# Performance work log

Measured on AMD Instinct MI355X. Metric: run time of the kernel, lower is better.

## Reference

```python
import jax, jax.numpy as jnp
import numpy as np

B, S, HID = 1, 2048, 2560
H, HKV, D = 32, 8, 128
G = H // HKV  # GQA group size = 4
EPS = 1e-6
THETA = 1000000.0


def _make_freqs_cis(seq_len, dim, theta):
    inv_freq = 1.0 / (theta ** (np.arange(0, dim, 2, dtype=np.float32) / dim))
    t = np.arange(seq_len, dtype=np.float32)
    ang = np.outer(t, inv_freq)  # [S, D/2]
    emb = np.concatenate([ang, ang], axis=-1)  # [S, D]
    return jnp.asarray(np.stack([np.cos(emb), np.sin(emb)], axis=0))  # [2, S, D]


def setup_inputs() -> dict:
    key = jax.random.key(0)
    ks = jax.random.split(key, 5)
    inp = {
        "hidden_states": jax.random.normal(ks[0], (B, S, HID), dtype=jnp.float32),
        "freqs_cis": _make_freqs_cis(S, D, THETA),
        "Wq": jax.random.normal(ks[1], (H * D, HID), dtype=jnp.float32) * 0.02,
        "Wk": jax.random.normal(ks[2], (HKV * D, HID), dtype=jnp.float32) * 0.02,
        "Wv": jax.random.normal(ks[3], (HKV * D, HID), dtype=jnp.float32) * 0.02,
        "Wo": jax.random.normal(ks[4], (HID, H * D), dtype=jnp.float32) * 0.02,
        "q_norm_w": jnp.ones((D,), dtype=jnp.float32),
        "k_norm_w": jnp.ones((D,), dtype=jnp.float32),
    }
    return inp


def _rms_norm(x, w):
    var = jnp.mean(jnp.square(x), axis=-1, keepdims=True)
    return x * jax.lax.rsqrt(var + EPS) * w


def _rotate_half(x):
    x1, x2 = jnp.split(x, 2, axis=-1)
    return jnp.concatenate([-x2, x1], axis=-1)


def reference(hidden_states, freqs_cis, Wq, Wk, Wv, Wo, q_norm_w, k_norm_w):
    # projections (torch Linear: x @ W.T)
    xq = jnp.einsum('bsh,oh->bso', hidden_states, Wq).reshape(B, S, H, D).swapaxes(1, 2)   # [B,H,S,D]
    xk = jnp.einsum('bsh,oh->bso', hidden_states, Wk).reshape(B, S, HKV, D).swapaxes(1, 2) # [B,Hkv,S,D]
    xv = jnp.einsum('bsh,oh->bso', hidden_states, Wv).reshape(B, S, HKV, D).swapaxes(1, 2)

    # per-head RMSNorm (gemma3-style q/k norm)
    xq = _rms_norm(xq, q_norm_w)
    xk = _rms_norm(xk, k_norm_w)

    # RoPE; cos/sin: [S,D] broadcasts over [B,H,S,D]
    cos, sin = freqs_cis[0], freqs_cis[1]
    xq = xq * cos + _rotate_half(xq) * sin
    xk = xk * cos + _rotate_half(xk) * sin

    # GQA attention without materializing repeated KV: group queries per kv head
    qg = xq.reshape(B, HKV, G, S, D)
    scores = jnp.einsum('bkgqd,bksd->bkgqs', qg, xk) / jnp.sqrt(jnp.asarray(D, xq.dtype))
    probs = jax.nn.softmax(scores, axis=-1)
    out = jnp.einsum('bkgqs,bksd->bkgqd', probs, xv)  # [B,Hkv,G,S,D]

    out = out.reshape(B, H, S, D).swapaxes(1, 2).reshape(B, S, H * D)
    return jnp.einsum('bso,ho->bsh', out, Wo)
```

## Files before the change

kernel.cpp:

```cpp
#include <hip/hip_runtime.h>
#include <stdint.h>

#define S_LEN 2048
#define HID   2560
#define NH    32
#define NKV   8
#define DH    128
#define QD    (NH*DH)
#define KVD   (NKV*DH)

typedef __attribute__((ext_vector_type(8)))  short          bf16x8;
typedef __attribute__((ext_vector_type(4)))  float          f32x4;
typedef __attribute__((ext_vector_type(16))) float          f32x16;
typedef __attribute__((ext_vector_type(8)))  unsigned short us8;

static __device__ __forceinline__ unsigned short f2bf(float f) {
  union { float f; uint32_t u; } v; v.f = f;
  uint32_t u = v.u;
  u += 0x7fff + ((u >> 16) & 1);
  return (unsigned short)(u >> 16);
}

static __device__ __forceinline__ void gload16(const void* g, void* l) {
  __builtin_amdgcn_global_load_lds(
      (const __attribute__((address_space(1))) uint32_t*)g,
      (__attribute__((address_space(3))) uint32_t*)l, 16, 0, 0);
}

static __device__ __forceinline__ unsigned cvtpk(float lo, float hi) {
  unsigned r;
  asm volatile("v_cvt_pk_bf16_f32 %0, %1, %2" : "=v"(r) : "v"(lo), "v"(hi));
  return r;
}

static __device__ __forceinline__ void plswap(unsigned& a, unsigned& b) {
  asm volatile("v_permlane32_swap_b32 %0, %1" : "+v"(a), "+v"(b));
}

__global__ void cast_bf16_k(const float* __restrict__ in,
                            unsigned short* __restrict__ out, int n4) {
  int stride = gridDim.x * blockDim.x;
  for (int i = blockIdx.x * blockDim.x + threadIdx.x; i < n4; i += stride) {
    float4 v = ((const float4*)in)[i];
    ushort4 o;
    o.x = f2bf(v.x); o.y = f2bf(v.y); o.z = f2bf(v.z); o.w = f2bf(v.w);
    ((ushort4*)out)[i] = o;
  }
}

#define BM 128
#define BN 128
#define BK 32

__global__ __launch_bounds__(256)
void gemm_bt(const unsigned short* __restrict__ A,
             const unsigned short* __restrict__ B,
             float* __restrict__ Cf, int M, int N, int K)
{
  __shared__ __align__(16) unsigned short sA[BM * BK];
  __shared__ __align__(16) unsigned short sB[BN * BK];
  const int tid  = threadIdx.x;
  const int wave = tid >> 6, lane = tid & 63;
  const int wr   = wave >> 1, wc = wave & 1;
  const int brow = blockIdx.y, bcol = blockIdx.x;
  const int l15  = lane & 15, lh = lane >> 4;

  f32x4 acc[4][4] = {};

  for (int k0 = 0; k0 < K; k0 += BK) {
    __syncthreads();
#pragma unroll
    for (int c = 0; c < 2; ++c) {
      int chunk = wave * 2 + c;
      int f = chunk * 512 + lane * 8;
      int row = f >> 5, col = f & 31;
      gload16(A + (size_t)(brow * BM + row) * K + k0 + col, (char*)sA + chunk * 1024);
      gload16(B + (size_t)(bcol * BN + row) * K + k0 + col, (char*)sB + chunk * 1024);
    }
    __syncthreads();

    bf16x8 af[4], bfr[4];
#pragma unroll
    for (int i = 0; i < 4; ++i)
      af[i] = *(const bf16x8*)((const char*)sA + (wr * 64 + i * 16 + l15) * 64 + lh * 16);
#pragma unroll
    for (int j = 0; j < 4; ++j)
      bfr[j] = *(const bf16x8*)((const char*)sB + (wc * 64 + j * 16 + l15) * 64 + lh * 16);
#pragma unroll
    for (int i = 0; i < 4; ++i)
#pragma unroll
      for (int j = 0; j < 4; ++j)
        acc[i][j] = __builtin_amdgcn_mfma_f32_16x16x32_bf16(af[i], bfr[j], acc[i][j], 0, 0, 0);
  }

#pragma unroll
  for (int i = 0; i < 4; ++i)
#pragma unroll
    for (int j = 0; j < 4; ++j) {
      int row = brow * BM + wr * 64 + i * 16 + lh * 4;
      int col = bcol * BN + wc * 64 + j * 16 + l15;
#pragma unroll
      for (int r = 0; r < 4; ++r)
        Cf[(size_t)(row + r) * N + col] = acc[i][j][r];
    }
}

__global__ __launch_bounds__(256)
void gemm_qkv(const unsigned short* __restrict__ A,
              const unsigned short* __restrict__ B,
              const float* __restrict__ freqs,
              const float* __restrict__ qw, const float* __restrict__ kw,
              unsigned short* __restrict__ Qo,
              unsigned short* __restrict__ Ko,
              unsigned short* __restrict__ Vo)
{
  __shared__ __align__(16) unsigned short sA[BM * BK];
  __shared__ __align__(16) unsigned short sB[BN * BK];
  const int tid  = threadIdx.x;
  const int wave = tid >> 6, lane = tid & 63;
  const int brow = blockIdx.y, bcol = blockIdx.x;
  const int l15  = lane & 15, lh = lane >> 4;

  f32x4 acc[2][8] = {};

  for (int k0 = 0; k0 < HID; k0 += BK) {
    __syncthreads();
#pragma unroll
    for (int c = 0; c < 2; ++c) {
      int chunk = wave * 2 + c;
      int f = chunk * 512 + lane * 8;
      int row = f >> 5, col = f & 31;
      gload16(A + (size_t)(brow * BM + row) * HID + k0 + col, (char*)sA + chunk * 1024);
      gload16(B + (size_t)(bcol * BN + row) * HID + k0 + col, (char*)sB + chunk * 1024);
    }
    __syncthreads();

    bf16x8 af[2], bfr[8];
#pragma unroll
    for (int i = 0; i < 2; ++i)
      af[i] = *(const bf16x8*)((const char*)sA + (wave * 32 + i * 16 + l15) * 64 + lh * 16);
#pragma unroll
    for (int j = 0; j < 8; ++j)
      bfr[j] = *(const bf16x8*)((const char*)sB + (j * 16 + l15) * 64 + lh * 16);
#pragma unroll
    for (int i = 0; i < 2; ++i)
#pragma unroll
      for (int j = 0; j < 8; ++j)
        acc[i][j] = __builtin_amdgcn_mfma_f32_16x16x32_bf16(af[i], bfr[j], acc[i][j], 0, 0, 0);
  }

  const int ncol0  = bcol * BN;
  const int region = (ncol0 < QD) ? 0 : (ncol0 < QD + KVD ? 1 : 2);
  const float* nw  = (region == 0) ? qw : kw;

#pragma unroll
  for (int i = 0; i < 2; ++i) {
#pragma unroll
    for (int r = 0; r < 4; ++r) {
      int s = brow * BM + wave * 32 + i * 16 + lh * 4 + r;
      float v[8];
#pragma unroll
      for (int j = 0; j < 8; ++j) v[j] = acc[i][j][r];
      if (region < 2) {
        float ss = 0.f;
#pragma unroll
        for (int j = 0; j < 8; ++j) ss += v[j] * v[j];
        ss += __shfl_xor(ss, 1); ss += __shfl_xor(ss, 2);
        ss += __shfl_xor(ss, 4); ss += __shfl_xor(ss, 8);
        float rsq = rsqrtf(ss * (1.0f / 128.0f) + 1e-6f);
        float y[8];
#pragma unroll
        for (int j = 0; j < 8; ++j) y[j] = v[j] * rsq * nw[j * 16 + l15];
        const float* cr = freqs + (size_t)s * DH;
        const float* sr = freqs + (size_t)(S_LEN + s) * DH;
#pragma unroll
        for (int j = 0; j < 4; ++j) {
          int d1 = j * 16 + l15, d2 = (j + 4) * 16 + l15;
          v[j]     = y[j]     * cr[d1] - y[j + 4] * sr[d1];
          v[j + 4] = y[j + 4] * cr[d2] + y[j]     * sr[d2];
        }
      }
      unsigned short* dst;
      if (region == 0)      dst = Qo + (size_t)s * QD  + ncol0;
      else if (region == 1) dst = Ko + (size_t)s * KVD + (ncol0 - QD);
      else                  dst = Vo + (size_t)s * KVD + (ncol0 - QD - KVD);
#pragma unroll
      for (int j = 0; j < 8; ++j) dst[j * 16 + l15] = f2bf(v[j]);
    }
  }
}

__global__ __launch_bounds__(256, 2)
void attn2_k(const unsigned short* __restrict__ Q,
             const unsigned short* __restrict__ Kb,
             const unsigned short* __restrict__ Vb,
             unsigned short* __restrict__ O)
{
  const float SC = 0.08838834764831845f * 1.4426950408889634f;
  __shared__ __align__(16) unsigned short sK[2][64 * 128];
  __shared__ __align__(16) unsigned short sV[2][128][72];

  const int kvh  = blockIdx.y;
  const int q0   = blockIdx.x * 32;
  const int wave = threadIdx.x >> 6, lane = threadIdx.x & 63;
  const int l31  = lane & 31, half = lane >> 5;
  const int h    = kvh * 4 + wave;
  const int vc0  = wave * 32;

  bf16x8 qf[8];
  {
    const unsigned short* qp = Q + (size_t)(q0 + l31) * QD + h * DH + half * 8;
#pragma unroll
    for (int ds = 0; ds < 8; ++ds) qf[ds] = *(const bf16x8*)(qp + ds * 16);
  }

  f32x16 oacc[4] = {};
  float m_c = -1e30f, l_c = 0.f;

  auto stageK = [&](int b, int t0) {
#pragma unroll
    for (int c = 0; c < 4; ++c) {
      int chunk = wave * 4 + c;
      int fb = chunk * 1024 + lane * 16;
      int row = fb >> 8;
      int gi = (fb & 255) ^ ((row & 7) << 4);
      gload16(Kb + (size_t)(t0 + row) * KVD + kvh * DH + (gi >> 1),
              (char*)sK[b] + chunk * 1024);
    }
  };
  auto loadV = [&](us8* vv, int t0) {
    const unsigned short* vsrc = Vb + (size_t)(t0 + lane) * KVD + kvh * DH + vc0;
#pragma unroll
    for (int u = 0; u < 4; ++u) vv[u] = *(const us8*)(vsrc + u * 8);
  };
  auto writeV = [&](int b, const us8* vv) {
#pragma unroll
    for (int u = 0; u < 4; ++u)
#pragma unroll
      for (int k = 0; k < 8; ++k)
        sV[b][vc0 + u * 8 + k][lane] = (unsigned short)vv[u][k];
  };

  {
    us8 vv[4];
    stageK(0, 0);
    loadV(vv, 0);
    writeV(0, vv);
  }
  asm volatile("s_waitcnt vmcnt(0)" ::: "memory");
  __syncthreads();
  int buf = 0;

  for (int t = 0; t < S_LEN / 64; ++t) {
    const bool pre = (t + 1 < S_LEN / 64);
    us8 vv[4];
    if (pre) { stageK(buf ^ 1, (t + 1) * 64); loadV(vv, (t + 1) * 64); }

    f32x16 sm[2] = {};
    __builtin_amdgcn_s_setprio(1);
#pragma unroll
    for (int kc = 0; kc < 2; ++kc) {
      int krow = kc * 32 + l31;
      int rb = krow * 256, sw = (krow & 7) << 4;
#pragma unroll
      for (int ds = 0; ds < 8; ++ds) {
        bf16x8 kf = *(const bf16x8*)((const char*)sK[buf] + rb + ((ds * 32 + half * 16) ^ sw));
        sm[kc] = __builtin_amdgcn_mfma_f32_32x32x16_bf16(kf, qf[ds], sm[kc], 0, 0, 0);
      }
    }
    __builtin_amdgcn_s_setprio(0);

    float mraw = sm[0][0];
#pragma unroll
    for (int kc = 0; kc < 2; ++kc)
#pragma unroll
      for (int r = 0; r < 16; ++r) mraw = fmaxf(mraw, sm[kc][r]);
    mraw = fmaxf(mraw, __shfl_xor(mraw, 32));
    float mn = fmaxf(m_c, mraw * SC);
    float corr = exp2f(m_c - mn);
    m_c = mn;

    float p[2][16];
    float sum = 0.f;
#pragma unroll
    for (int kc = 0; kc < 2; ++kc)
#pragma unroll
      for (int r = 0; r < 16; ++r) {
        p[kc][r] = exp2f(sm[kc][r] * SC - mn);
        sum += p[kc][r];
      }
    sum += __shfl_xor(sum, 32);
    l_c = l_c * corr + sum;

    bf16x8 pfrag[4];
#pragma unroll
    for (int kc = 0; kc < 2; ++kc)
#pragma unroll
      for (int ksl = 0; ksl < 2; ++ksl) {
        int rb = ksl * 8;
        unsigned x0 = cvtpk(p[kc][rb + 0], p[kc][rb + 1]);
        unsigned y0 = cvtpk(p[kc][rb + 4], p[kc][rb + 5]);
        unsigned x1 = cvtpk(p[kc][rb + 2], p[kc][rb + 3]);
        unsigned y1 = cvtpk(p[kc][rb + 6], p[kc][rb + 7]);
        plswap(x0, y0);
        plswap(x1, y1);
        union { unsigned w[4]; bf16x8 v; } u;
        u.w[0] = x0; u.w[1] = x1; u.w[2] = y0; u.w[3] = y1;
        pfrag[kc * 2 + ksl] = u.v;
      }

    if (pre) writeV(buf ^ 1, vv);

#pragma unroll
    for (int dt = 0; dt < 4; ++dt)
#pragma unroll
      for (int r = 0; r < 16; ++r) oacc[dt][r] *= corr;

    __builtin_amdgcn_s_setprio(1);
#pragma unroll
    for (int dt = 0; dt < 4; ++dt) {
#pragma unroll
      for (int ks = 0; ks < 4; ++ks) {
        bf16x8 vfa = *(const bf16x8*)&sV[buf][dt * 32 + l31][ks * 16 + half * 8];
        oacc[dt] = __builtin_amdgcn_mfma_f32_32x32x16_bf16(vfa, pfrag[ks], oacc[dt], 0, 0, 0);
      }
    }
    __builtin_amdgcn_s_setprio(0);

    asm volatile("s_waitcnt vmcnt(0)" ::: "memory");
    __syncthreads();
    buf ^= 1;
  }

  {
    float inv = 1.0f / l_c;
    unsigned short* orow = O + (size_t)(q0 + l31) * QD + h * DH;
#pragma unroll
    for (int dt = 0; dt < 4; ++dt)
#pragma unroll
      for (int r = 0; r < 16; r += 2) {
        int d = dt * 32 + (r & 3) + 8 * (r >> 2) + 4 * half;
        unsigned w = cvtpk(oacc[dt][r] * inv, oacc[dt][r + 1] * inv);
        *(unsigned*)(orow + d) = w;
      }
  }
}

extern "C" void kernel_launch(void* const* d_in, const int* in_sizes, int n_in,
                              void* d_out, int out_size, void* d_ws, size_t ws_size,
                              hipStream_t stream)
{
  const float* hs    = (const float*)d_in[0];
  const float* freqs = (const float*)d_in[1];
  const float* Wq    = (const float*)d_in[2];
  const float* Wk    = (const float*)d_in[3];
  const float* Wv    = (const float*)d_in[4];
  const float* Wo    = (const float*)d_in[5];
  const float* qw    = (const float*)d_in[6];
  const float* kw    = (const float*)d_in[7];
  float* out = (float*)d_out;

  char* ws = (char*)d_ws;
  size_t off = 0;
  auto alloc = [&](size_t bytes) {
    char* p = ws + off;
    off += (bytes + 255) & ~(size_t)255;
    return p;
  };
  unsigned short* hs_b   = (unsigned short*)alloc((size_t)S_LEN * HID * 2);
  unsigned short* wqkv_b = (unsigned short*)alloc((size_t)(QD + 2 * KVD) * HID * 2);
  unsigned short* Wo_b   = (unsigned short*)alloc((size_t)HID * QD * 2);
  unsigned short* q_b    = (unsigned short*)alloc((size_t)S_LEN * QD * 2);
  unsigned short* k_b    = (unsigned short*)alloc((size_t)S_LEN * KVD * 2);
  unsigned short* v_b    = (unsigned short*)alloc((size_t)S_LEN * KVD * 2);
  unsigned short* at_b   = (unsigned short*)alloc((size_t)S_LEN * QD * 2);

  auto cast = [&](const float* src, unsigned short* dst, int n) {
    int n4 = n / 4;
    int blocks = (n4 + 255) / 256; if (blocks > 2048) blocks = 2048;
    cast_bf16_k<<<dim3(blocks), dim3(256), 0, stream>>>(src, dst, n4);
  };
  cast(hs, hs_b, S_LEN * HID);
  cast(Wq, wqkv_b,                       QD * HID);
  cast(Wk, wqkv_b + (size_t)QD * HID,    KVD * HID);
  cast(Wv, wqkv_b + (size_t)(QD + KVD) * HID, KVD * HID);
  cast(Wo, Wo_b, HID * QD);

  gemm_qkv<<<dim3((QD + 2 * KVD) / BN, S_LEN / BM), dim3(256), 0, stream>>>(
      hs_b, wqkv_b, freqs, qw, kw, q_b, k_b, v_b);

  attn2_k<<<dim3(S_LEN / 32, NKV), dim3(256), 0, stream>>>(q_b, k_b, v_b, at_b);

  gemm_bt<<<dim3(HID / BN, S_LEN / BM), dim3(256), 0, stream>>>(
      at_b, Wo_b, out, S_LEN, HID, QD);
}
```

Baseline: 501.6 us.

## Merge cast kernels, double GEMM K-tile with XOR-swizzled LDS, remap workgroups

Replaces the five per-tensor fp32-to-bf16 cast launches with one kernel that writes into the contiguous workspace, which relies on the workspace buffers being laid out back-to-back with 256-byte alignment. Both GEMMs move from a K-tile of 32 to 64 with an XOR swizzle on the LDS layout, to halve the number of barrier-bounded iterations and to avoid bank conflicts on fragment reads. Workgroup IDs are also remapped across groups of eight, with the intent of improving L2 reuse. The larger tile doubles LDS use per block.

```diff
diff --git a/kernel.cpp b/kernel.cpp
--- a/kernel.cpp
+++ b/kernel.cpp
@@ -37,20 +37,37 @@
   asm volatile("v_permlane32_swap_b32 %0, %1" : "+v"(a), "+v"(b));
 }
 
-__global__ void cast_bf16_k(const float* __restrict__ in,
-                            unsigned short* __restrict__ out, int n4) {
+#define N_HS4 1310720
+#define B0 1310720
+#define B1 3932160
+#define B2 4587520
+#define B3 5242880
+#define B4 7864320
+
+__global__ void cast_all_k(const float* __restrict__ hs,
+                           const float* __restrict__ Wq,
+                           const float* __restrict__ Wk,
+                           const float* __restrict__ Wv,
+                           const float* __restrict__ Wo,
+                           ushort4* __restrict__ dst) {
   int stride = gridDim.x * blockDim.x;
-  for (int i = blockIdx.x * blockDim.x + threadIdx.x; i < n4; i += stride) {
-    float4 v = ((const float4*)in)[i];
+  for (int i = blockIdx.x * blockDim.x + threadIdx.x; i < B4; i += stride) {
+    const float* s; int rel;
+    if (i < B0)      { s = hs; rel = i; }
+    else if (i < B1) { s = Wq; rel = i - B0; }
+    else if (i < B2) { s = Wk; rel = i - B1; }
+    else if (i < B3) { s = Wv; rel = i - B2; }
+    else             { s = Wo; rel = i - B3; }
+    float4 v = ((const float4*)s)[rel];
     ushort4 o;
     o.x = f2bf(v.x); o.y = f2bf(v.y); o.z = f2bf(v.z); o.w = f2bf(v.w);
-    ((ushort4*)out)[i] = o;
+    dst[i] = o;
   }
 }
 
 #define BM 128
 #define BN 128
-#define BK 32
+#define BK 64
 
 __global__ __launch_bounds__(256)
 void gemm_bt(const unsigned short* __restrict__ A,
@@ -62,35 +79,49 @@
   const int tid  = threadIdx.x;
   const int wave = tid >> 6, lane = tid & 63;
   const int wr   = wave >> 1, wc = wave & 1;
-  const int brow = blockIdx.y, bcol = blockIdx.x;
   const int l15  = lane & 15, lh = lane >> 4;
+
+  const int nwg = gridDim.x * gridDim.y;
+  const int wg  = blockIdx.y * gridDim.x + blockIdx.x;
+  const int swz = (wg & 7) * (nwg >> 3) + (wg >> 3);
+  const int bcol = swz % gridDim.x, brow = swz / gridDim.x;
 
   f32x4 acc[4][4] = {};
 
   for (int k0 = 0; k0 < K; k0 += BK) {
     __syncthreads();
 #pragma unroll
-    for (int c = 0; c < 2; ++c) {
-      int chunk = wave * 2 + c;
-      int f = chunk * 512 + lane * 8;
-      int row = f >> 5, col = f & 31;
-      gload16(A + (size_t)(brow * BM + row) * K + k0 + col, (char*)sA + chunk * 1024);
-      gload16(B + (size_t)(bcol * BN + row) * K + k0 + col, (char*)sB + chunk * 1024);
+    for (int c = 0; c < 4; ++c) {
+      int fb  = (wave * 4 + c) * 1024;
+      int db  = fb + lane * 16;
+      int row = db >> 7;
+      int gi  = (db & 127) ^ ((row & 7) << 4);
+      gload16(A + (size_t)(brow * BM + row) * K + k0 + (gi >> 1), (char*)sA + fb);
+      gload16(B + (size_t)(bcol * BN + row) * K + k0 + (gi >> 1), (char*)sB + fb);
     }
     __syncthreads();
 
-    bf16x8 af[4], bfr[4];
-#pragma unroll
-    for (int i = 0; i < 4; ++i)
-      af[i] = *(const bf16x8*)((const char*)sA + (wr * 64 + i * 16 + l15) * 64 + lh * 16);
-#pragma unroll
-    for (int j = 0; j < 4; ++j)
-      bfr[j] = *(const bf16x8*)((const char*)sB + (wc * 64 + j * 16 + l15) * 64 + lh * 16);
-#pragma unroll
-    for (int i = 0; i < 4; ++i)
-#pragma unroll
-      for (int j = 0; j < 4; ++j)
-        acc[i][j] = __builtin_amdgcn_mfma_f32_16x16x32_bf16(af[i], bfr[j], acc[i][j], 0, 0, 0);
+#pragma unroll
+    for (int ks = 0; ks < 2; ++ks) {
+      bf16x8 af[4], bfr[4];
+#pragma unroll
+      for (int i = 0; i < 4; ++i) {
+        int row = wr * 64 + i * 16 + l15;
+        af[i] = *(const bf16x8*)((const char*)sA + row * 128 +
+                                 ((ks * 64 + lh * 16) ^ ((row & 7) << 4)));
+      }
+#pragma unroll
+      for (int j = 0; j < 4; ++j) {
+        int row = wc * 64 + j * 16 + l15;
+        bfr[j] = *(const bf16x8*)((const char*)sB + row * 128 +
+                                  ((ks * 64 + lh * 16) ^ ((row & 7) << 4)));
+      }
+#pragma unroll
+      for (int i = 0; i < 4; ++i)
+#pragma unroll
+        for (int j = 0; j < 4; ++j)
+          acc[i][j] = __builtin_amdgcn_mfma_f32_16x16x32_bf16(af[i], bfr[j], acc[i][j], 0, 0, 0);
+    }
   }
 
 #pragma unroll
@@ -118,35 +149,49 @@
   __shared__ __align__(16) unsigned short sB[BN * BK];
   const int tid  = threadIdx.x;
   const int wave = tid >> 6, lane = tid & 63;
-  const int brow = blockIdx.y, bcol = blockIdx.x;
   const int l15  = lane & 15, lh = lane >> 4;
+
+  const int nwg = gridDim.x * gridDim.y;
+  const int wg  = blockIdx.y * gridDim.x + blockIdx.x;
+  const int swz = (wg & 7) * (nwg >> 3) + (wg >> 3);
+  const int bcol = swz % gridDim.x, brow = swz / gridDim.x;
 
   f32x4 acc[2][8] = {};
 
   for (int k0 = 0; k0 < HID; k0 += BK) {
     __syncthreads();
 #pragma unroll
-    for (int c = 0; c < 2; ++c) {
-      int chunk = wave * 2 + c;
-      int f = chunk * 512 + lane * 8;
-      int row = f >> 5, col = f & 31;
-      gload16(A + (size_t)(brow * BM + row) * HID + k0 + col, (char*)sA + chunk * 1024);
-      gload16(B + (size_t)(bcol * BN + row) * HID + k0 + col, (char*)sB + chunk * 1024);
+    for (int c = 0; c < 4; ++c) {
+      int fb  = (wave * 4 + c) * 1024;
+      int db  = fb + lane * 16;
+      int row = db >> 7;
+      int gi  = (db & 127) ^ ((row & 7) << 4);
+      gload16(A + (size_t)(brow * BM + row) * HID + k0 + (gi >> 1), (char*)sA + fb);
+      gload16(B + (size_t)(bcol * BN + row) * HID + k0 + (gi >> 1), (char*)sB + fb);
     }
     __syncthreads();
 
-    bf16x8 af[2], bfr[8];
-#pragma unroll
-    for (int i = 0; i < 2; ++i)
-      af[i] = *(const bf16x8*)((const char*)sA + (wave * 32 + i * 16 + l15) * 64 + lh * 16);
-#pragma unroll
-    for (int j = 0; j < 8; ++j)
-      bfr[j] = *(const bf16x8*)((const char*)sB + (j * 16 + l15) * 64 + lh * 16);
-#pragma unroll
-    for (int i = 0; i < 2; ++i)
-#pragma unroll
-      for (int j = 0; j < 8; ++j)
-        acc[i][j] = __builtin_amdgcn_mfma_f32_16x16x32_bf16(af[i], bfr[j], acc[i][j], 0, 0, 0);
+#pragma unroll
+    for (int ks = 0; ks < 2; ++ks) {
+      bf16x8 af[2], bfr[8];
+#pragma unroll
+      for (int i = 0; i < 2; ++i) {
+        int row = wave * 32 + i * 16 + l15;
+        af[i] = *(const bf16x8*)((const char*)sA + row * 128 +
+                                 ((ks * 64 + lh * 16) ^ ((row & 7) << 4)));
+      }
+#pragma unroll
+      for (int j = 0; j < 8; ++j) {
+        int row = j * 16 + l15;
+        bfr[j] = *(const bf16x8*)((const char*)sB + row * 128 +
+                                  ((ks * 64 + lh * 16) ^ ((row & 7) << 4)));
+      }
+#pragma unroll
+      for (int i = 0; i < 2; ++i)
+#pragma unroll
+        for (int j = 0; j < 8; ++j)
+          acc[i][j] = __builtin_amdgcn_mfma_f32_16x16x32_bf16(af[i], bfr[j], acc[i][j], 0, 0, 0);
+    }
   }
 
   const int ncol0  = bcol * BN;
@@ -375,16 +420,7 @@
   unsigned short* v_b    = (unsigned short*)alloc((size_t)S_LEN * KVD * 2);
   unsigned short* at_b   = (unsigned short*)alloc((size_t)S_LEN * QD * 2);
 
-  auto cast = [&](const float* src, unsigned short* dst, int n) {
-    int n4 = n / 4;
-    int blocks = (n4 + 255) / 256; if (blocks > 2048) blocks = 2048;
-    cast_bf16_k<<<dim3(blocks), dim3(256), 0, stream>>>(src, dst, n4);
-  };
-  cast(hs, hs_b, S_LEN * HID);
-  cast(Wq, wqkv_b,                       QD * HID);
-  cast(Wk, wqkv_b + (size_t)QD * HID,    KVD * HID);
-  cast(Wv, wqkv_b + (size_t)(QD + KVD) * HID, KVD * HID);
-  cast(Wo, Wo_b, HID * QD);
+  cast_all_k<<<dim3(4096), dim3(256), 0, stream>>>(hs, Wq, Wk, Wv, Wo, (ushort4*)hs_b);
 
   gemm_qkv<<<dim3((QD + 2 * KVD) / BN, S_LEN / BM), dim3(256), 0, stream>>>(
       hs_b, wqkv_b, freqs, qw, kw, q_b, k_b, v_b);
```

Result: faster. 458.1 us (-8.7%).
